# Performance work log

Measured on AMD Instinct MI355X. Metric: run time of the kernel, lower is better.

Reference implementation:

```python
import jax, jax.numpy as jnp
import numpy as np
from jax import lax

H_IMG, W_IMG = 1280, 1280
STRIDES = (8, 16, 32, 64, 128)
FEAT_SHAPES = tuple((H_IMG // s) * (W_IMG // s) for s in STRIDES)  # (25600,6400,1600,400,100)
N_POINTS = sum(FEAT_SHAPES)  # 34100
NUM_CLASSES = 1
TOPK = 1000
SCORE_THRESH = 0.05
NMS_THRESH = 0.5
MAX_DET = 300
BATCH = 8
N_GT = 200


def make_points():
    # matches AnchorFreePS.reference_points: cell centers at stride*i + stride//2, (cx, cy) order
    pts = []
    for s in STRIDES:
        h, w = H_IMG // s, W_IMG // s
        cx = np.arange(w, dtype=np.float32) * s + s // 2
        cy = np.arange(h, dtype=np.float32) * s + s // 2
        gy, gx = np.meshgrid(cy, cx, indexing='ij')
        pts.append(np.stack([gx, gy], axis=-1).reshape(-1, 2))
    return jnp.asarray(np.concatenate(pts, axis=0))


def setup_inputs() -> dict:
    key = jax.random.key(0)
    k1, k2, k3, k4 = jax.random.split(key, 4)
    points = make_points()  # [N,2]
    xy = jax.random.uniform(k1, (BATCH, N_GT, 2), minval=0.0, maxval=1000.0)
    wh = jax.random.uniform(k2, (BATCH, N_GT, 2), minval=20.0, maxval=260.0)
    gt_boxes = jnp.concatenate([xy, xy + wh], axis=-1)  # [B,M,4] x1y1x2y2
    cls_logits = jax.random.normal(k3, (BATCH, N_POINTS, NUM_CLASSES)) * 1.5 - 3.0
    regression = jax.random.uniform(k4, (BATCH, N_POINTS, 4)) * 0.1  # normalized ltrb codes
    return {"points": points, "gt_boxes": gt_boxes, "cls_logits": cls_logits, "regression": regression}


def match_points_to_boxes(points, gt_boxes):
    # point-in-box test + area-cost argmin (compute_loss matched_idxs)
    px = points[None, :, None, 0]  # [1,N,1]
    py = points[None, :, None, 1]
    b = gt_boxes[:, None, :, :]    # [B,1,M,4]
    inside = (px >= b[..., 0]) & (px <= b[..., 2]) & (py >= b[..., 1]) & (py <= b[..., 3])  # [B,N,M]
    matched = jnp.any(inside, axis=-1)  # [B,N]
    areas = (gt_boxes[..., 2] - gt_boxes[..., 0]) * (gt_boxes[..., 3] - gt_boxes[..., 1])  # [B,M]
    BIG = jnp.float32(2 ** 31 - 1)  # torch.iinfo(torch.int).max
    cost = jnp.where(inside, areas[:, None, :], BIG)
    idx = jnp.argmin(cost, axis=-1)
    return jnp.where(matched, idx, -1)


def decode_boxes(rel, pts):
    # FCOSBoxCoder.decode_single with weights (1,1,1,1)
    l = rel[:, 0] * W_IMG
    t = rel[:, 1] * H_IMG
    r = rel[:, 2] * W_IMG
    b = rel[:, 3] * H_IMG
    x, y = pts[:, 0], pts[:, 1]
    return jnp.stack([x - l, y - t, x + r, y + b], axis=-1)


def clip_boxes(boxes):
    return jnp.stack([
        jnp.clip(boxes[:, 0], 0.0, W_IMG),
        jnp.clip(boxes[:, 1], 0.0, H_IMG),
        jnp.clip(boxes[:, 2], 0.0, W_IMG),
        jnp.clip(boxes[:, 3], 0.0, H_IMG)], axis=-1)


def nms(boxes, scores, labels, valid_init):
    # fixed-size sequential NMS equivalent to batched_nms (same-label suppression)
    work = lax.stop_gradient(jnp.where(valid_init, scores, -jnp.inf))

    def body(w, _):
        i = jnp.argmax(w)
        s = w[i]
        box = boxes[i]
        x1 = jnp.maximum(box[0], boxes[:, 0])
        y1 = jnp.maximum(box[1], boxes[:, 1])
        x2 = jnp.minimum(box[2], boxes[:, 2])
        y2 = jnp.minimum(box[3], boxes[:, 3])
        inter = jnp.clip(x2 - x1, 0.0) * jnp.clip(y2 - y1, 0.0)
        a1 = (box[2] - box[0]) * (box[3] - box[1])
        a2 = (boxes[:, 2] - boxes[:, 0]) * (boxes[:, 3] - boxes[:, 1])
        iou = inter / (a1 + a2 - inter + 1e-9)
        supp = (iou > NMS_THRESH) & (labels == labels[i])
        w = jnp.where(supp, -jnp.inf, w).at[i].set(-jnp.inf)
        return w, (i, s)

    _, (idxs, picked) = lax.scan(body, work, None, length=MAX_DET)
    valid = picked > -jnp.inf
    return idxs, valid


def postprocess_image(points, cls_i, reg_i):
    bx_list, sc_list, lb_list = [], [], []
    off = 0
    for size in FEAT_SHAPES:  # fixed small level loop
        sl = slice(off, off + size)
        off += size
        scores = jax.nn.sigmoid(cls_i[sl]).reshape(-1)  # [size*C]
        k = min(TOPK, size * NUM_CLASSES)
        sc, idx = lax.top_k(scores, k)
        a = idx // NUM_CLASSES
        lb = idx % NUM_CLASSES
        bx = clip_boxes(decode_boxes(reg_i[sl][a], points[sl][a]))
        bx_list.append(bx)
        sc_list.append(sc)
        lb_list.append(lb)
    boxes = jnp.concatenate(bx_list, axis=0)
    scores = jnp.concatenate(sc_list, axis=0)
    labels = jnp.concatenate(lb_list, axis=0)
    idxs, valid = nms(boxes, scores, labels, scores > SCORE_THRESH)
    out_boxes = jnp.where(valid[:, None], boxes[idxs], 0.0)
    out_scores = jnp.where(valid, scores[idxs], 0.0)
    out_labels = jnp.where(valid, labels[idxs], -1)
    return out_boxes, out_scores, out_labels, valid


def reference(points, gt_boxes, cls_logits, regression):
    matched_idxs = match_points_to_boxes(points, gt_boxes)  # [B,N]
    boxes, scores, labels, valid = jax.vmap(
        lambda c, r: postprocess_image(points, c, r))(cls_logits, regression)
    return matched_idxs, boxes, scores, labels, valid
```

## Files before the change

kernel.cpp:

```cpp
#include <hip/hip_runtime.h>
#include <stdint.h>

#define N_POINTS   34100
#define BATCH      8
#define N_GT       200
#define NLEV       5
#define NCAND      3500
#define MAX_DET    300
#define SCORE_TH   0.05f
#define NMS_TH     0.5f
#define IMG        1280.0f
#define NBIN       4096
#define TIE_CAP    4096
#define MTH 0.50000002980232238769531250

#define OUT_MATCH  0
#define OUT_BOXES  272800
#define OUT_SCORES 282400
#define OUT_LABELS 284800
#define OUT_VALID  287200

#define WS_KEYS    0
#define WS_PARAMS  1746560
#define WS_SBOX    2632192
#define WS_SSC     3080192
#define WS_MASK    3192192
#define WS_DIAG    9500032
#define MASK_STRIDE 98560
#define DIAG_STRIDE 3520

typedef unsigned long long u64;
typedef uint32_t u32;

__device__ __forceinline__ int mask_off(int c) {
    int g = c >> 6;
    return 64 * (55 * g - (g * (g - 1)) / 2) + (c - (g << 6)) * (55 - g);
}

__device__ __forceinline__ int level_of(int p) {
    return (p < 25600) ? 0 : (p < 32000) ? 1 : (p < 33600) ? 2 : (p < 34000) ? 3 : 4;
}
__device__ __forceinline__ int loff_of(int l) {
    return (l == 0) ? 0 : (l == 1) ? 25600 : (l == 2) ? 32000 : (l == 3) ? 33600 : 34000;
}
__device__ __forceinline__ int lsize_of(int l) {
    return (l == 0) ? 25600 : (l == 1) ? 6400 : (l == 2) ? 1600 : (l == 3) ? 400 : 100;
}
__device__ __forceinline__ int k_of(int l) {
    return (l == 0) ? 1000 : (l == 1) ? 1000 : (l == 2) ? 1000 : (l == 3) ? 400 : 100;
}
__device__ __forceinline__ u64 readlane64(u64 v, int t) {
    u32 lo = (u32)__builtin_amdgcn_readlane((int)(u32)v, t);
    u32 hi = (u32)__builtin_amdgcn_readlane((int)(u32)(v >> 32), t);
    return ((u64)hi << 32) | lo;
}

#define MPT 2
__global__ __launch_bounds__(256)
void match_key_kernel(const float* __restrict__ points,
                      const float* __restrict__ gt,
                      const float* __restrict__ logits,
                      float* __restrict__ out_match,
                      u32* __restrict__ keys) {
#pragma clang fp contract(off)
    __shared__ float bx1[N_GT], by1[N_GT], bx2[N_GT], by2[N_GT], ar[N_GT];
    const int b = blockIdx.y;
    const int base = blockIdx.x * (256 * MPT) + threadIdx.x;

    for (int j = threadIdx.x; j < N_GT; j += 256) {
        float x1 = gt[(b * N_GT + j) * 4 + 0];
        float y1 = gt[(b * N_GT + j) * 4 + 1];
        float x2 = gt[(b * N_GT + j) * 4 + 2];
        float y2 = gt[(b * N_GT + j) * 4 + 3];
        bx1[j] = x1; by1[j] = y1; bx2[j] = x2; by2[j] = y2;
        ar[j] = (x2 - x1) * (y2 - y1);
    }
    __syncthreads();

    const float BIGF = 2147483648.0f;
    float px[MPT], py[MPT], best[MPT];
    int bi[MPT];
#pragma unroll
    for (int k = 0; k < MPT; ++k) {
        int p = base + k * 256;
        int pc = (p < N_POINTS) ? p : 0;
        px[k] = points[pc * 2 + 0];
        py[k] = points[pc * 2 + 1];
        best[k] = BIGF; bi[k] = -1;
    }
    for (int j = 0; j < N_GT; ++j) {
        float x1 = bx1[j], y1 = by1[j], x2 = bx2[j], y2 = by2[j], a = ar[j];
#pragma unroll
        for (int k = 0; k < MPT; ++k) {
            bool inside = (px[k] >= x1) && (px[k] <= x2) &&
                          (py[k] >= y1) && (py[k] <= y2);
            float cost = inside ? a : BIGF;
            if (cost < best[k]) { best[k] = cost; bi[k] = j; }
        }
    }
#pragma unroll
    for (int k = 0; k < MPT; ++k) {
        int p = base + k * 256;
        if (p >= N_POINTS) continue;
        out_match[b * N_POINTS + p] = (float)bi[k];
        float lg = logits[b * N_POINTS + p];
        float s = 1.0f / (1.0f + expf(-lg));
        u32 u = __float_as_uint(s);
        u32 key = (u & 0x80000000u) ? ~u : (u | 0x80000000u);
        keys[b * N_POINTS + p] = key;
    }
}

__global__ __launch_bounds__(256)
void hist_select_kernel(const u32* __restrict__ keys,
                        u32* __restrict__ params) {
    __shared__ u32 h[NBIN];
    const int seg = blockIdx.x;
    const int b = seg / NLEV;
    const int l = seg - b * NLEV;
    const int tid = threadIdx.x;

    for (int i = tid; i < NBIN; i += 256) h[i] = 0u;
    __syncthreads();

    const u32* k = keys + b * N_POINTS + loff_of(l);
    const int n = lsize_of(l);
    for (int i = tid; i < n; i += 256)
        atomicAdd(&h[(k[i] >> 19) & 4095u], 1u);
    __syncthreads();

    if (tid < 64) {
        const u32 K = (u32)k_of(l);
        const int lane = tid;
        u32 S = 0;
#pragma unroll 8
        for (int i = 0; i < 64; ++i) S += h[lane * 64 + i];
        u32 acc = S;
#pragma unroll
        for (int off = 1; off < 64; off <<= 1) {
            u32 v = (u32)__shfl_down((int)acc, off);
            if (lane + off < 64) acc += v;
        }
        u32 sfxAfter = acc - S;
        bool hit = (sfxAfter < K) && (sfxAfter + S >= K);
        u64 bal = __ballot(hit);
        int Lg = (int)__builtin_ctzll(bal);
        u32 sfxG = (u32)__shfl((int)sfxAfter, Lg);

        u32 v = h[Lg * 64 + lane];
        u32 acc2 = v;
#pragma unroll
        for (int off = 1; off < 64; off <<= 1) {
            u32 t = (u32)__shfl_down((int)acc2, off);
            if (lane + off < 64) acc2 += t;
        }
        u32 sfx2 = sfxG + acc2 - v;
        bool hit2 = (sfx2 < K) && (sfx2 + v >= K);
        if (hit2) {
            params[seg * 2 + 0] = (u32)(Lg * 64 + lane);
            params[seg * 2 + 1] = K - sfx2;
        }
    }
}

#define SORT_T 1024
__global__ __launch_bounds__(SORT_T)
void pipeline_kernel(const u32* __restrict__ keys,
                     const u32* __restrict__ params,
                     const float* __restrict__ reg,
                     const float* __restrict__ points,
                     float* __restrict__ sboxes,
                     float* __restrict__ sscores) {
#pragma clang fp contract(off)
    __shared__ u64 sk[4096];
    __shared__ u64 tb[TIE_CAP];
    __shared__ u64 aux[4096];
    __shared__ u32 h[NBIN];
    __shared__ u32 bs[NBIN];
    __shared__ u32 sTl[NLEV], skkl[NLEV], wt[16];
    __shared__ u32 scnt, stcnt;

    const int b = blockIdx.x;
    const int tid = threadIdx.x;
    const int lane = tid & 63;
    const int wid = tid >> 6;
    const u32* kk_ = keys + b * N_POINTS;

    if (tid < NLEV) {
        sTl[tid]  = params[(b * NLEV + tid) * 2 + 0];
        skkl[tid] = params[(b * NLEV + tid) * 2 + 1];
    }
    if (tid == 0) { scnt = 0u; stcnt = 0u; }
    __syncthreads();

    const int NPAIR = N_POINTS / 2;
    for (int i0 = tid; i0 - tid < NPAIR; i0 += SORT_T) {
        bool act = i0 < NPAIR;
        int p0 = act ? (2 * i0) : 0;
        int p1 = p0 + 1;
        u32 key0 = kk_[p0], key1 = kk_[p1];
        int l0 = level_of(p0), l1 = level_of(p1);
        u32 d0 = (key0 >> 19) & 4095u, d1 = (key1 >> 19) & 4095u;
        u32 T0 = sTl[l0], T1 = sTl[l1];
        bool def0 = act && (d0 > T0), def1 = act && (d1 > T1);
        bool tie0 = act && (d0 == T0), tie1 = act && (d1 == T1);
        u64 k0 = ((u64)key0 << 18) | ((u64)(7 - l0) << 15)
               | (u64)(32767 - (p0 - loff_of(l0)));
        u64 k1 = ((u64)key1 << 18) | ((u64)(7 - l1) << 15)
               | (u64)(32767 - (p1 - loff_of(l1)));

        u32 nd = (u32)def0 + (u32)def1;
        u32 pre = nd;
#pragma unroll
        for (int off = 1; off < 64; off <<= 1) {
            u32 v = (u32)__shfl_up((int)pre, off);
            if (lane >= off) pre += v;
        }
        u32 base_ = 0;
        if (lane == 63 && pre) base_ = atomicAdd(&scnt, pre);
        base_ = (u32)__shfl((int)base_, 63);
        u32 ex = pre - nd;
        if (def0) sk[base_ + ex] = k0;
        if (def1) sk[base_ + ex + (u32)def0] = k1;

        u32 nt = (u32)tie0 + (u32)tie1;
        u32 pret = nt;
#pragma unroll
        for (int off = 1; off < 64; off <<= 1) {
            u32 v = (u32)__shfl_up((int)pret, off);
            if (lane >= off) pret += v;
        }
        u32 baset = 0;
        if (lane == 63 && pret) baset = atomicAdd(&stcnt, pret);
        baset = (u32)__shfl((int)baset, 63);
        u32 ext = pret - nt;
        if (tie0 && baset + ext < TIE_CAP) tb[baset + ext] = k0;
        if (tie1 && baset + ext + (u32)tie0 < TIE_CAP)
            tb[baset + ext + (u32)tie0] = k1;
    }
    __syncthreads();

    const u64 below = (lane == 0) ? 0ull : (~0ull >> (64 - lane));
    int t = (int)stcnt; if (t > TIE_CAP) t = TIE_CAP;
    for (int j0 = tid; j0 - tid < t; j0 += SORT_T) {
        bool active = j0 < t;
        u64 kj = active ? tb[j0] : 0ull;
        u32 lvtag = (u32)(kj >> 15) & 7u;
        int r = 0;
        for (int i = 0; i < t; ++i) {
            u64 ki = tb[i];
            r += (ki > kj && (((u32)(ki >> 15) & 7u) == lvtag)) ? 1 : 0;
        }
        bool inc = active && (r < (int)skkl[7 - lvtag]);
        u64 grp = __ballot(inc);
        if (grp) {
            int leader = (int)__builtin_ctzll(grp);
            u32 base_ = 0;
            if (lane == leader)
                base_ = atomicAdd(&scnt, (u32)__builtin_popcountll(grp));
            base_ = (u32)__shfl((int)base_, leader);
            if (inc) sk[base_ + (u32)__builtin_popcountll(grp & below)] = kj;
        }
    }
    __syncthreads();
    const int total = (int)scnt;

    for (int i = tid; i < NBIN; i += SORT_T) h[i] = 0u;
    __syncthreads();
    for (int i = tid; i < total; i += SORT_T)
        atomicAdd(&h[(u32)(sk[i] >> 37) & 4095u], 1u);
    __syncthreads();

    u32 t0 = h[4095 - 4 * tid];
    u32 t1 = h[4095 - (4 * tid + 1)];
    u32 t2 = h[4095 - (4 * tid + 2)];
    u32 t3 = h[4095 - (4 * tid + 3)];
    u32 tsum = t0 + t1 + t2 + t3;
    u32 sc_ = tsum;
#pragma unroll
    for (int off = 1; off < 64; off <<= 1) {
        u32 v = (u32)__shfl_up((int)sc_, off);
        if (lane >= off) sc_ += v;
    }
    if (lane == 63) wt[wid] = sc_;
    __syncthreads();
    if (tid < 64) {
        u32 v = (tid < 16) ? wt[tid] : 0u;
        u32 s2 = v;
#pragma unroll
        for (int off = 1; off < 16; off <<= 1) {
            u32 x = (u32)__shfl_up((int)s2, off);
            if (tid >= off) s2 += x;
        }
        if (tid < 16) wt[tid] = s2 - v;
    }
    __syncthreads();
    u32 run = (sc_ - tsum) + wt[wid];
    bs[4095 - 4 * tid] = run;       run += t0;
    bs[4095 - (4 * tid + 1)] = run; run += t1;
    bs[4095 - (4 * tid + 2)] = run; run += t2;
    bs[4095 - (4 * tid + 3)] = run;
    __syncthreads();
    for (int i = tid; i < NBIN; i += SORT_T) h[i] = 0u;
    __syncthreads();
    for (int i = tid; i < total; i += SORT_T) {
        u64 k = sk[i];
        u32 d = (u32)(k >> 37) & 4095u;
        u32 pos = bs[d] + atomicAdd(&h[d], 1u);
        aux[pos] = k;
    }
    __syncthreads();
    for (int p = tid; p < total; p += SORT_T) {
        u64 kp = aux[p];
        u32 d = (u32)(kp >> 37) & 4095u;
        u32 gbase = bs[d];
        u32 gend = (d == 0) ? (u32)total : bs[d - 1];
        u32 r = 0;
        for (u32 q = gbase; q < gend; ++q) r += (aux[q] > kp) ? 1u : 0u;
        sk[gbase + r] = kp;
    }
    __syncthreads();

    for (int r = tid; r < NCAND; r += SORT_T) {
        float x1 = 0.f, y1 = 0.f, x2 = 0.f, y2 = 0.f, sc = 0.f;
        if (r < total) {
            u64 k50 = sk[r];
            int lowb = (int)(k50 & 0x3FFFFull);
            int l = 7 - (lowb >> 15);
            int idxl = 32767 - (lowb & 32767);
            int p = loff_of(l) + idxl;
            u32 key32 = (u32)(k50 >> 18);
            sc = __uint_as_float(key32 ^ 0x80000000u);
            int gp = b * N_POINTS + p;
            float l_ = reg[gp * 4 + 0] * IMG;
            float t_ = reg[gp * 4 + 1] * IMG;
            float r_ = reg[gp * 4 + 2] * IMG;
            float bb = reg[gp * 4 + 3] * IMG;
            float px = points[p * 2 + 0];
            float py = points[p * 2 + 1];
            x1 = fminf(fmaxf(px - l_, 0.0f), IMG);
            y1 = fminf(fmaxf(py - t_, 0.0f), IMG);
            x2 = fminf(fmaxf(px + r_, 0.0f), IMG);
            y2 = fminf(fmaxf(py + bb, 0.0f), IMG);
        }
        int slot = b * NCAND + r;
        sboxes[slot * 4 + 0] = x1;
        sboxes[slot * 4 + 1] = y1;
        sboxes[slot * 4 + 2] = x2;
        sboxes[slot * 4 + 3] = y2;
        sscores[slot] = sc;
    }
}

__global__ __launch_bounds__(256)
void mask_kernel(const float* __restrict__ sboxes,
                 const float* __restrict__ sscores,
                 u64* __restrict__ mask,
                 u64* __restrict__ diag) {
#pragma clang fp contract(off)
    const int b = blockIdx.y;
    const int wv = threadIdx.x >> 6;
    const int lane = threadIdx.x & 63;
    const int NG = (NCAND + 3) >> 2;
    const int NH = (NG + 1) >> 1;
    const int gidx = blockIdx.x * 4 + wv;
    if (gidx >= NH) return;

    const float4* gb = (const float4*)sboxes + b * NCAND;
    const float* gs = sscores + b * NCAND;
    u64* mout = mask + (size_t)b * MASK_STRIDE;
    u64* dout = diag + (size_t)b * DIAG_STRIDE;

    for (int s = 0; s < 2; ++s) {
        const int g0 = (s == 0) ? gidx : (NG - 1 - gidx);
        if (s == 1 && g0 == gidx) break;
        const int c0 = g0 << 2;

        float4 bc[4]; float a1[4]; bool ok[4]; int g[4]; u64* rp[4];
        bool any = false;
#pragma unroll
        for (int i = 0; i < 4; ++i) {
            int c = c0 + i;
            int cc = (c < NCAND) ? c : (NCAND - 1);
            bc[i] = gb[cc];
            a1[i] = (bc[i].z - bc[i].x) * (bc[i].w - bc[i].y);
            ok[i] = (c < NCAND) && (gs[cc] > SCORE_TH);
            g[i] = cc >> 6;
            rp[i] = mout + mask_off(cc) - g[i];
            any |= ok[i];
        }
        if (!any) continue;

        for (int w = (c0 >> 6); w < 55; ++w) {
            int cj = (w << 6) + lane;
            float4 bj = (cj < NCAND) ? gb[cj] : make_float4(0.f, 0.f, 0.f, 0.f);
            float a2 = (bj.z - bj.x) * (bj.w - bj.y);
#pragma unroll
            for (int i = 0; i < 4; ++i) {
                float x1 = fmaxf(bc[i].x, bj.x);
                float y1 = fmaxf(bc[i].y, bj.y);
                float x2 = fminf(bc[i].z, bj.z);
                float y2 = fminf(bc[i].w, bj.w);
                float inter = fmaxf(x2 - x1, 0.f) * fmaxf(y2 - y1, 0.f);
                float denom = a1[i] + a2 - inter + 1e-9f;
                float hf = 0.5f * denom;
                float rr = fmaf(0x1p-25f, denom, hf);
                u64 bits = __ballot(inter > rr);
                u64 eq = __ballot(inter == rr);
                if (eq) {
                    u64 fb = __ballot((double)inter > MTH * (double)denom);
                    bits |= (eq & fb);
                }
                if (lane == 0 && ok[i] && w >= g[i]) {
                    rp[i][w] = bits;
                    if (w == g[i]) dout[c0 + i] = bits;
                }
            }
        }
    }
}

__global__ __launch_bounds__(64)
void scan_kernel(const float* __restrict__ sboxes,
                 const float* __restrict__ sscores,
                 const u64* __restrict__ mask,
                 const u64* __restrict__ diag,
                 float* __restrict__ out) {
    const int b = blockIdx.x;
    const int lane = threadIdx.x;
    const float4* gb = (const float4*)sboxes + b * NCAND;
    const float* gs = sscores + b * NCAND;
    const u64* mrow = mask + (size_t)b * MASK_STRIDE;
    const u64* drow = diag + (size_t)b * DIAG_STRIDE;

    float* ob = out + OUT_BOXES  + b * MAX_DET * 4;
    float* os = out + OUT_SCORES + b * MAX_DET;
    float* ol = out + OUT_LABELS + b * MAX_DET;
    float* ov = out + OUT_VALID  + b * MAX_DET;

    u64 m = 0ull;
    u64 rowN = drow[lane];
    float4 bjN = gb[lane];
    float sjN = gs[lane];

    int kept = 0;
    for (int w = 0; w < 55; ++w) {
        const int wbase = w << 6;
        const u64 row = rowN;
        const float4 bj = bjN;
        const float sj = sjN;
        if (w < 54) {
            int cn = wbase + 64 + lane;
            int cc = (cn < NCAND) ? cn : (NCAND - 1);
            rowN = drow[cc];
            bjN = gb[cc];
            float s = gs[cc];
            sjN = (cn < NCAND) ? s : 0.f;
        }
        int c = wbase + lane;
        u64 bad = __ballot(!((c < NCAND) && (sj > SCORE_TH)));
        u64 cur = readlane64(m, w) | bad;
        u64 km = 0ull;
        while (kept < MAX_DET) {
            u64 avail = ~cur;
            if (avail == 0ull) break;
            int t = (int)__builtin_ctzll(avail);
            u64 r = readlane64(row, t);
            cur |= r | (1ull << t);
            km |= 1ull << t;
            if (lane == t) {
                ob[kept * 4 + 0] = bj.x;
                ob[kept * 4 + 1] = bj.y;
                ob[kept * 4 + 2] = bj.z;
                ob[kept * 4 + 3] = bj.w;
                os[kept] = sj;
                ol[kept] = 0.0f;
                ov[kept] = 1.0f;
            }
            kept++;
        }
        if (km) {
            const bool lr = (lane >= w && lane < 55);
            const int lo = lane - w;
            u64 acc = 0ull;
            while (km) {
#define POPBIT(tn) int tn = -1; if (km) { tn = (int)__builtin_ctzll(km); km &= km - 1ull; }
                POPBIT(t0) POPBIT(t1) POPBIT(t2) POPBIT(t3)
                POPBIT(t4) POPBIT(t5) POPBIT(t6) POPBIT(t7)
#undef POPBIT
                u64 v0 = 0, v1 = 0, v2 = 0, v3 = 0, v4 = 0, v5 = 0, v6 = 0, v7 = 0;
                if (lr) {
                    v0 = mrow[mask_off(wbase + t0) + lo];
                    if (t1 >= 0) v1 = mrow[mask_off(wbase + t1) + lo];
                    if (t2 >= 0) v2 = mrow[mask_off(wbase + t2) + lo];
                    if (t3 >= 0) v3 = mrow[mask_off(wbase + t3) + lo];
                    if (t4 >= 0) v4 = mrow[mask_off(wbase + t4) + lo];
                    if (t5 >= 0) v5 = mrow[mask_off(wbase + t5) + lo];
                    if (t6 >= 0) v6 = mrow[mask_off(wbase + t6) + lo];
                    if (t7 >= 0) v7 = mrow[mask_off(wbase + t7) + lo];
                }
                acc |= ((v0 | v1) | (v2 | v3)) | ((v4 | v5) | (v6 | v7));
            }
            m |= acc;
        }
        if (kept >= MAX_DET) break;
    }
    for (int k = kept + lane; k < MAX_DET; k += 64) {
        ob[k * 4 + 0] = 0.f; ob[k * 4 + 1] = 0.f;
        ob[k * 4 + 2] = 0.f; ob[k * 4 + 3] = 0.f;
        os[k] = 0.f; ol[k] = -1.f; ov[k] = 0.f;
    }
}

extern "C" void kernel_launch(void* const* d_in, const int* in_sizes, int n_in,
                              void* d_out, int out_size, void* d_ws, size_t ws_size,
                              hipStream_t stream) {
    const float* points = (const float*)d_in[0];
    const float* gt     = (const float*)d_in[1];
    const float* logits = (const float*)d_in[2];
    const float* reg    = (const float*)d_in[3];
    float* out = (float*)d_out;

    u32* keys      = (u32*)((char*)d_ws + WS_KEYS);
    u32* params    = (u32*)((char*)d_ws + WS_PARAMS);
    float* sboxes  = (float*)((char*)d_ws + WS_SBOX);
    float* sscores = (float*)((char*)d_ws + WS_SSC);
    u64* mask   = (u64*)((char*)d_ws + WS_MASK);
    u64* diag   = (u64*)((char*)d_ws + WS_DIAG);

    dim3 g1((N_POINTS + 256 * MPT - 1) / (256 * MPT), BATCH);
    match_key_kernel<<<g1, 256, 0, stream>>>(points, gt, logits,
                                             out + OUT_MATCH, keys);

    hist_select_kernel<<<BATCH * NLEV, 256, 0, stream>>>(keys, params);

    pipeline_kernel<<<BATCH, SORT_T, 0, stream>>>(keys, params, reg, points,
                                                  sboxes, sscores);

    dim3 g5((((NCAND + 3) / 4 + 1) / 2 + 3) / 4, BATCH);
    mask_kernel<<<g5, 256, 0, stream>>>(sboxes, sscores, mask, diag);

    scan_kernel<<<BATCH, 64, 0, stream>>>(sboxes, sscores, mask, diag, out);
}
```

Before: 280.6 us.

## Fuse matching and histogram-select kernels into one heterogeneous launch

Merges the point-to-box matching kernel and the per-level histogram threshold kernel into a single launch, with the block index choosing the role. The histogram blocks now compute sigmoid keys from the logits themselves and bin them directly, so they no longer depend on the matching blocks and the two jobs run side by side. This removes one kernel launch and its inter-kernel dependency gap, and drops the re-read of keys. In exchange each histogram block does the sigmoid work serially over a whole level, and shared memory is sized for the larger of the two roles.

```diff
diff --git a/kernel.cpp b/kernel.cpp
--- a/kernel.cpp
+++ b/kernel.cpp
@@ -36,7 +36,6 @@
     int g = c >> 6;
     return 64 * (55 * g - (g * (g - 1)) / 2) + (c - (g << 6)) * (55 - g);
 }
-
 __device__ __forceinline__ int level_of(int p) {
     return (p < 25600) ? 0 : (p < 32000) ? 1 : (p < 33600) ? 2 : (p < 34000) ? 3 : 4;
 }
@@ -56,109 +55,117 @@
 }
 
 #define MPT 2
+#define MATCH_BLKS 536
+#define FRONT_BLKS (MATCH_BLKS + BATCH * NLEV)
+
 __global__ __launch_bounds__(256)
-void match_key_kernel(const float* __restrict__ points,
-                      const float* __restrict__ gt,
-                      const float* __restrict__ logits,
-                      float* __restrict__ out_match,
-                      u32* __restrict__ keys) {
+void front_kernel(const float* __restrict__ points,
+                  const float* __restrict__ gt,
+                  const float* __restrict__ logits,
+                  float* __restrict__ out_match,
+                  u32* __restrict__ keys,
+                  u32* __restrict__ params) {
 #pragma clang fp contract(off)
-    __shared__ float bx1[N_GT], by1[N_GT], bx2[N_GT], by2[N_GT], ar[N_GT];
-    const int b = blockIdx.y;
-    const int base = blockIdx.x * (256 * MPT) + threadIdx.x;
-
-    for (int j = threadIdx.x; j < N_GT; j += 256) {
-        float x1 = gt[(b * N_GT + j) * 4 + 0];
-        float y1 = gt[(b * N_GT + j) * 4 + 1];
-        float x2 = gt[(b * N_GT + j) * 4 + 2];
-        float y2 = gt[(b * N_GT + j) * 4 + 3];
-        bx1[j] = x1; by1[j] = y1; bx2[j] = x2; by2[j] = y2;
-        ar[j] = (x2 - x1) * (y2 - y1);
-    }
-    __syncthreads();
-
-    const float BIGF = 2147483648.0f;
-    float px[MPT], py[MPT], best[MPT];
-    int bi[MPT];
-#pragma unroll
-    for (int k = 0; k < MPT; ++k) {
-        int p = base + k * 256;
-        int pc = (p < N_POINTS) ? p : 0;
-        px[k] = points[pc * 2 + 0];
-        py[k] = points[pc * 2 + 1];
-        best[k] = BIGF; bi[k] = -1;
-    }
-    for (int j = 0; j < N_GT; ++j) {
-        float x1 = bx1[j], y1 = by1[j], x2 = bx2[j], y2 = by2[j], a = ar[j];
+    __shared__ __align__(16) u32 shm[NBIN];
+    const int tid = threadIdx.x;
+
+    if (blockIdx.x < MATCH_BLKS) {
+        float* bx1 = (float*)shm;
+        float* by1 = bx1 + 256;
+        float* bx2 = bx1 + 512;
+        float* by2 = bx1 + 768;
+        float* ar  = bx1 + 1024;
+        const int b = blockIdx.x / 67;
+        const int chunk = blockIdx.x - b * 67;
+        const int base = chunk * (256 * MPT) + tid;
+
+        for (int j = tid; j < N_GT; j += 256) {
+            float x1 = gt[(b * N_GT + j) * 4 + 0];
+            float y1 = gt[(b * N_GT + j) * 4 + 1];
+            float x2 = gt[(b * N_GT + j) * 4 + 2];
+            float y2 = gt[(b * N_GT + j) * 4 + 3];
+            bx1[j] = x1; by1[j] = y1; bx2[j] = x2; by2[j] = y2;
+            ar[j] = (x2 - x1) * (y2 - y1);
+        }
+        __syncthreads();
+
+        const float BIGF = 2147483648.0f;
+        float px[MPT], py[MPT], best[MPT];
+        int bi[MPT];
 #pragma unroll
         for (int k = 0; k < MPT; ++k) {
-            bool inside = (px[k] >= x1) && (px[k] <= x2) &&
-                          (py[k] >= y1) && (py[k] <= y2);
-            float cost = inside ? a : BIGF;
-            if (cost < best[k]) { best[k] = cost; bi[k] = j; }
-        }
-    }
-#pragma unroll
-    for (int k = 0; k < MPT; ++k) {
-        int p = base + k * 256;
-        if (p >= N_POINTS) continue;
-        out_match[b * N_POINTS + p] = (float)bi[k];
-        float lg = logits[b * N_POINTS + p];
-        float s = 1.0f / (1.0f + expf(-lg));
-        u32 u = __float_as_uint(s);
-        u32 key = (u & 0x80000000u) ? ~u : (u | 0x80000000u);
-        keys[b * N_POINTS + p] = key;
-    }
-}
-
-__global__ __launch_bounds__(256)
-void hist_select_kernel(const u32* __restrict__ keys,
-                        u32* __restrict__ params) {
-    __shared__ u32 h[NBIN];
-    const int seg = blockIdx.x;
-    const int b = seg / NLEV;
-    const int l = seg - b * NLEV;
-    const int tid = threadIdx.x;
-
-    for (int i = tid; i < NBIN; i += 256) h[i] = 0u;
-    __syncthreads();
-
-    const u32* k = keys + b * N_POINTS + loff_of(l);
-    const int n = lsize_of(l);
-    for (int i = tid; i < n; i += 256)
-        atomicAdd(&h[(k[i] >> 19) & 4095u], 1u);
-    __syncthreads();
-
-    if (tid < 64) {
-        const u32 K = (u32)k_of(l);
-        const int lane = tid;
-        u32 S = 0;
+            int p = base + k * 256;
+            int pc = (p < N_POINTS) ? p : 0;
+            px[k] = points[pc * 2 + 0];
+            py[k] = points[pc * 2 + 1];
+            best[k] = BIGF; bi[k] = -1;
+        }
+        for (int j = 0; j < N_GT; ++j) {
+            float x1 = bx1[j], y1 = by1[j], x2 = bx2[j], y2 = by2[j], a = ar[j];
+#pragma unroll
+            for (int k = 0; k < MPT; ++k) {
+                bool inside = (px[k] >= x1) && (px[k] <= x2) &&
+                              (py[k] >= y1) && (py[k] <= y2);
+                float cost = inside ? a : BIGF;
+                if (cost < best[k]) { best[k] = cost; bi[k] = j; }
+            }
+        }
+#pragma unroll
+        for (int k = 0; k < MPT; ++k) {
+            int p = base + k * 256;
+            if (p < N_POINTS) out_match[b * N_POINTS + p] = (float)bi[k];
+        }
+    } else {
+        const int seg = blockIdx.x - MATCH_BLKS;
+        const int b = seg / NLEV;
+        const int l = seg - b * NLEV;
+        const int lane = tid & 63;
+
+        for (int i = tid; i < NBIN; i += 256) shm[i] = 0u;
+        __syncthreads();
+
+        const float* lg = logits + b * N_POINTS + loff_of(l);
+        u32* kout = keys + b * N_POINTS + loff_of(l);
+        const int n = lsize_of(l);
+        for (int i = tid; i < n; i += 256) {
+            float s = 1.0f / (1.0f + expf(-lg[i]));
+            u32 u = __float_as_uint(s);
+            u32 key = (u & 0x80000000u) ? ~u : (u | 0x80000000u);
+            kout[i] = key;
+            atomicAdd(&shm[(key >> 19) & 4095u], 1u);
+        }
+        __syncthreads();
+
+        if (tid < 64) {
+            const u32 K = (u32)k_of(l);
+            u32 S = 0;
 #pragma unroll 8
-        for (int i = 0; i < 64; ++i) S += h[lane * 64 + i];
-        u32 acc = S;
-#pragma unroll
-        for (int off = 1; off < 64; off <<= 1) {
-            u32 v = (u32)__shfl_down((int)acc, off);
-            if (lane + off < 64) acc += v;
-        }
-        u32 sfxAfter = acc - S;
-        bool hit = (sfxAfter < K) && (sfxAfter + S >= K);
-        u64 bal = __ballot(hit);
-        int Lg = (int)__builtin_ctzll(bal);
-        u32 sfxG = (u32)__shfl((int)sfxAfter, Lg);
-
-        u32 v = h[Lg * 64 + lane];
-        u32 acc2 = v;
-#pragma unroll
-        for (int off = 1; off < 64; off <<= 1) {
-            u32 t = (u32)__shfl_down((int)acc2, off);
-            if (lane + off < 64) acc2 += t;
-        }
-        u32 sfx2 = sfxG + acc2 - v;
-        bool hit2 = (sfx2 < K) && (sfx2 + v >= K);
-        if (hit2) {
-            params[seg * 2 + 0] = (u32)(Lg * 64 + lane);
-            params[seg * 2 + 1] = K - sfx2;
+            for (int i = 0; i < 64; ++i) S += shm[lane * 64 + i];
+            u32 acc = S;
+#pragma unroll
+            for (int off = 1; off < 64; off <<= 1) {
+                u32 v = (u32)__shfl_down((int)acc, off);
+                if (lane + off < 64) acc += v;
+            }
+            u32 sfxAfter = acc - S;
+            bool hit = (sfxAfter < K) && (sfxAfter + S >= K);
+            u64 bal = __ballot(hit);
+            int Lg = (int)__builtin_ctzll(bal);
+            u32 sfxG = (u32)__shfl((int)sfxAfter, Lg);
+
+            u32 v = shm[Lg * 64 + lane];
+            u32 acc2 = v;
+#pragma unroll
+            for (int off = 1; off < 64; off <<= 1) {
+                u32 t = (u32)__shfl_down((int)acc2, off);
+                if (lane + off < 64) acc2 += t;
+            }
+            u32 sfx2 = sfxG + acc2 - v;
+            bool hit2 = (sfx2 < K) && (sfx2 + v >= K);
+            if (hit2) {
+                params[seg * 2 + 0] = (u32)(Lg * 64 + lane);
+                params[seg * 2 + 1] = K - sfx2;
+            }
         }
     }
 }
@@ -528,11 +535,8 @@
     u64* mask   = (u64*)((char*)d_ws + WS_MASK);
     u64* diag   = (u64*)((char*)d_ws + WS_DIAG);
 
-    dim3 g1((N_POINTS + 256 * MPT - 1) / (256 * MPT), BATCH);
-    match_key_kernel<<<g1, 256, 0, stream>>>(points, gt, logits,
-                                             out + OUT_MATCH, keys);
-
-    hist_select_kernel<<<BATCH * NLEV, 256, 0, stream>>>(keys, params);
+    front_kernel<<<FRONT_BLKS, 256, 0, stream>>>(points, gt, logits,
+                                                 out + OUT_MATCH, keys, params);
 
     pipeline_kernel<<<BATCH, SORT_T, 0, stream>>>(keys, params, reg, points,
                                                   sboxes, sscores);
```

Measured after the change: 270.7 us. -3.5%, faster.
